# Kernel tuning notes

Measured on AMD Instinct MI355X. Metric: run time of the kernel, lower is better.

## Reference

```python
import jax, jax.numpy as jnp
import numpy as np
from jax.ops import segment_sum

NUM_HEADS = 16
NEG_INF = -jnp.inf


def setup_inputs() -> dict:
    key = jax.random.key(0)
    ks = jax.random.split(key, 12)
    D, H = 1024, NUM_HEADS
    SRC, TGT = 2048, 2048
    V, EV = 32000, 2000
    s = 1.0 / np.sqrt(D)
    return {
        "logits": jax.random.normal(ks[0], (TGT, V), jnp.float32),
        "extended_vocab_ids": jax.random.randint(ks[1], (SRC,), 0, V + EV, jnp.int32),
        "src_subtokens": jax.random.normal(ks[2], (SRC, D), jnp.float32),
        "tgt_subtokens": jax.random.normal(ks[3], (TGT, D), jnp.float32),
        "w_q": jax.random.normal(ks[4], (D, D), jnp.float32) * s,
        "b_q": jax.random.normal(ks[5], (D,), jnp.float32) * 0.02,
        "w_k": jax.random.normal(ks[6], (D, D), jnp.float32) * s,
        "b_k": jax.random.normal(ks[7], (D,), jnp.float32) * 0.02,
        "w_ptr": jax.random.normal(ks[8], (D,), jnp.float32) * s,
        "b_ptr": jax.random.normal(ks[9], (1,), jnp.float32) * 0.02,
        "len_vocab": V,
        "len_extended_vocab": EV,
    }


def _mha_attention(query, key, w_q, b_q, w_k, b_k):
    # SimpleMHA.unbatched_forward: project q/k, per-head scaled dot-product
    # softmax over src, mean over heads -> [TGT, SRC]
    TGT, D = query.shape
    SRC = key.shape[0]
    hd = D // NUM_HEADS
    q = (query @ w_q.T + b_q).reshape(TGT, NUM_HEADS, hd)
    k = (key @ w_k.T + b_k).reshape(SRC, NUM_HEADS, hd)
    scores = jnp.einsum("thd,shd->hts", q, k) / jnp.sqrt(jnp.float32(hd))
    attn = jax.nn.softmax(scores, axis=-1)  # [H, TGT, SRC]
    return attn.mean(axis=0)  # [TGT, SRC]


def reference(logits, extended_vocab_ids, src_subtokens, tgt_subtokens,
              w_q, b_q, w_k, b_k, w_ptr, b_ptr, len_vocab, len_extended_vocab):
    total = len_vocab + len_extended_vocab
    eps = jnp.finfo(jnp.float32).eps
    fmin = jnp.finfo(jnp.float32).min

    # copy gate: sigmoid(Linear(tgt)) -> [TGT, 1]
    copy_prob = jax.nn.sigmoid(tgt_subtokens @ w_ptr + b_ptr[0])[:, None]

    # attention distribution over src tokens [TGT, SRC]
    attn = _mha_attention(tgt_subtokens, src_subtokens, w_q, b_q, w_k, b_k)

    # attention @ one-hot(M) == scatter-add of attention columns by vocab id
    attn_vocab = segment_sum(attn.T, extended_vocab_ids, num_segments=total).T  # [TGT, total]
    attn_vocab = jnp.where(attn_vocab == 0, eps, attn_vocab)
    pointer_log_probs = jnp.log(attn_vocab)

    decoder_log_probs = jax.nn.log_softmax(logits, axis=1)
    decoder_log_probs = jnp.pad(decoder_log_probs, ((0, 0), (0, len_extended_vocab)),
                                constant_values=NEG_INF)

    p = jnp.stack([decoder_log_probs + jnp.log(1.0 - copy_prob),
                   pointer_log_probs + jnp.log(copy_prob)])
    p = jnp.where(p == NEG_INF, fmin, p)
    return jax.scipy.special.logsumexp(p, axis=0)
```

## Files before the change

### kernel.cpp

```cpp
#include <hip/hip_runtime.h>

typedef __attribute__((ext_vector_type(8))) short short8;
typedef __attribute__((ext_vector_type(4))) float f32x4;
typedef __attribute__((ext_vector_type(4))) unsigned int u32x4;
typedef unsigned short u16;
typedef unsigned int u32;

#define MFMA16 __builtin_amdgcn_mfma_f32_16x16x32_bf16

static constexpr int TGT = 2048, SRCN = 2048, DIM = 1024, NH = 16;
static constexpr int NV = 32000, NTOT = 34000;
#define FLT_EPS 1.1920928955078125e-07f

__device__ __forceinline__ u16 f2bf(float f) {
  unsigned u = __float_as_uint(f);
  return (u16)((u + 0x7FFFu + ((u >> 16) & 1u)) >> 16);
}

__device__ __forceinline__ int swz8(int row, int seg) {
  return row * 64 + ((seg ^ (row & 7)) << 3);
}

__device__ __forceinline__ void stats_row_body(
    int t, const float* __restrict__ logits, const float* __restrict__ tgt,
    const float* __restrict__ w_ptr, const float* __restrict__ b_ptr,
    float4* __restrict__ rowc, int tid, int lane, int w, float* red) {
  const f32x4* l4 = (const f32x4*)(logits + (size_t)t * NV);
  float e0 = 0.f, e1 = 0.f, e2 = 0.f, e3 = 0.f;
  const f32x4 z4 = {0.f, 0.f, 0.f, 0.f};
#pragma unroll 2
  for (int pk = 0; pk < 8; ++pk) {
    int g0 = pk * 1024 + tid;
    int g1 = g0 + 256, g2 = g0 + 512, g3 = g0 + 768;
    bool d0 = g0 < NV / 4, d1 = g1 < NV / 4, d2 = g2 < NV / 4, d3 = g3 < NV / 4;
    f32x4 v0 = d0 ? l4[g0] : z4;
    f32x4 v1 = d1 ? l4[g1] : z4;
    f32x4 v2 = d2 ? l4[g2] : z4;
    f32x4 v3 = d3 ? l4[g3] : z4;
    float s0 = (__expf(v0.x) + __expf(v0.y)) + (__expf(v0.z) + __expf(v0.w));
    float s1 = (__expf(v1.x) + __expf(v1.y)) + (__expf(v1.z) + __expf(v1.w));
    float s2 = (__expf(v2.x) + __expf(v2.y)) + (__expf(v2.z) + __expf(v2.w));
    float s3 = (__expf(v3.x) + __expf(v3.y)) + (__expf(v3.z) + __expf(v3.w));
    e0 += d0 ? s0 : 0.f;
    e1 += d1 ? s1 : 0.f;
    e2 += d2 ? s2 : 0.f;
    e3 += d3 ? s3 : 0.f;
  }
  float es = (e0 + e1) + (e2 + e3);

  float4 xv = *(const float4*)&tgt[(size_t)t * DIM + tid * 4];
  float4 wv = *(const float4*)&w_ptr[tid * 4];
  float g = (xv.x * wv.x + xv.y * wv.y) + (xv.z * wv.z + xv.w * wv.w);
  for (int d = 1; d < 64; d <<= 1) {
    es += __shfl_xor(es, d, 64);
    g += __shfl_xor(g, d, 64);
  }
  if (lane == 0) { red[w] = es; red[4 + w] = g; }
  __syncthreads();
  if (tid == 0) {
    float tot = red[0] + red[1] + red[2] + red[3];
    float gs = red[4] + red[5] + red[6] + red[7] + b_ptr[0];
    float c = 1.0f / (1.0f + __expf(-gs));
    float4 rc;
    rc.x = (1.0f - c) / tot;
    rc.y = c * FLT_EPS;
    rc.z = c;
    rc.w = 0.f;
    rowc[t] = rc;
  }
}

__device__ __forceinline__ void sort_body(
    const int* __restrict__ ids, int* __restrict__ sperm,
    u32* __restrict__ segmap, u32* __restrict__ ustart,
    int tid, int lane, int w, char* smem) {
  int* kk_ = (int*)smem;
  int* vv_ = (int*)(smem + 8192);
  int* scan = (int*)(smem + 16384);
  for (int i = tid; i < 2048; i += 256) { kk_[i] = ids[i]; vv_[i] = i; }
  for (int i = tid; i < 2048; i += 256) ustart[i] = 0xFFFFFFFFu;
  if (tid == 0) scan[4] = 0;
  __syncthreads();
  for (int kk = 2; kk <= 2048; kk <<= 1)
    for (int j = kk >> 1; j > 0; j >>= 1) {
      for (int m = tid; m < 1024; m += 256) {
        int i = ((m & ~(j - 1)) << 1) | (m & (j - 1));
        int l = i | j;
        bool asc = ((i & kk) == 0);
        int ki = kk_[i], kl = kk_[l];
        if ((ki > kl) == asc) {
          kk_[i] = kl; kk_[l] = ki;
          int tv = vv_[i]; vv_[i] = vv_[l]; vv_[l] = tv;
        }
      }
      __syncthreads();
    }
  for (int i = tid; i < 2048; i += 256) sperm[i] = vv_[i];
  for (int i = tid; i < NTOT; i += 256) segmap[i] = 0xFFFFFFFFu;
  __syncthreads();
  for (int c = 0; c < 8; ++c) {
    int p = c * 256 + tid;
    int id = kk_[p];
    bool head = (p == 0) || (kk_[p - 1] != id);
    unsigned long long bal = __ballot(head);
    int lanepfx = __popcll(bal & ((1ull << lane) - 1ull));
    int wtot = __popcll(bal);
    if (lane == 0) scan[w] = wtot;
    __syncthreads();
    int woff = 0;
    for (int i = 0; i < w; ++i) woff += scan[i];
    int base = scan[4];
    if (head) {
      int q = p + 1;
      while (q < 2048 && kk_[q] == id) ++q;
      int rank = base + woff + lanepfx;
      u32 cnt = (u32)(q - p);
      segmap[id] = (u32)rank | (cnt << 16);
      ustart[rank] = (u32)p | (cnt << 16);
    }
    __syncthreads();
    if (tid == 0) scan[4] = base + scan[0] + scan[1] + scan[2] + scan[3];
    __syncthreads();
  }
}

__global__ __launch_bounds__(256) void proj_gemm(
    const float* __restrict__ Xq, const float* __restrict__ Wq,
    const float* __restrict__ Bq, u16* __restrict__ Cq,
    const float* __restrict__ Xk, const float* __restrict__ Wk,
    const float* __restrict__ Bk, u16* __restrict__ Ck) {
  const int zz = blockIdx.z;
  const float* X = zz ? Xk : Xq;
  const float* W = zz ? Wk : Wq;
  const float* bias = zz ? Bk : Bq;
  u16* C = zz ? Ck : Cq;
  const float scale = zz ? 1.0f : 0.125f;

  __shared__ u16 As[128 * 32];
  __shared__ u16 Bs[128 * 32];
  const int n0 = blockIdx.x * 128, m0 = blockIdx.y * 128;
  const int tid = threadIdx.x, lane = tid & 63, w = tid >> 6;
  const int wr = w >> 1, wc = w & 1;
  const int srow = tid >> 1, shalf = tid & 1;
  f32x4 acc[4][4] = {};

  for (int k0 = 0; k0 < DIM; k0 += 32) {
    __syncthreads();
    {
      const float* pa = X + (size_t)(m0 + srow) * DIM + k0 + shalf * 16;
      const float* pb = W + (size_t)(n0 + srow) * DIM + k0 + shalf * 16;
      float4 a0 = ((const float4*)pa)[0], a1 = ((const float4*)pa)[1];
      float4 a2 = ((const float4*)pa)[2], a3 = ((const float4*)pa)[3];
      float4 b0 = ((const float4*)pb)[0], b1 = ((const float4*)pb)[1];
      float4 b2 = ((const float4*)pb)[2], b3 = ((const float4*)pb)[3];
      short8 wa0, wa1, wb0, wb1;
      wa0[0]=(short)f2bf(a0.x); wa0[1]=(short)f2bf(a0.y); wa0[2]=(short)f2bf(a0.z); wa0[3]=(short)f2bf(a0.w);
      wa0[4]=(short)f2bf(a1.x); wa0[5]=(short)f2bf(a1.y); wa0[6]=(short)f2bf(a1.z); wa0[7]=(short)f2bf(a1.w);
      wa1[0]=(short)f2bf(a2.x); wa1[1]=(short)f2bf(a2.y); wa1[2]=(short)f2bf(a2.z); wa1[3]=(short)f2bf(a2.w);
      wa1[4]=(short)f2bf(a3.x); wa1[5]=(short)f2bf(a3.y); wa1[6]=(short)f2bf(a3.z); wa1[7]=(short)f2bf(a3.w);
      wb0[0]=(short)f2bf(b0.x); wb0[1]=(short)f2bf(b0.y); wb0[2]=(short)f2bf(b0.z); wb0[3]=(short)f2bf(b0.w);
      wb0[4]=(short)f2bf(b1.x); wb0[5]=(short)f2bf(b1.y); wb0[6]=(short)f2bf(b1.z); wb0[7]=(short)f2bf(b1.w);
      wb1[0]=(short)f2bf(b2.x); wb1[1]=(short)f2bf(b2.y); wb1[2]=(short)f2bf(b2.z); wb1[3]=(short)f2bf(b2.w);
      wb1[4]=(short)f2bf(b3.x); wb1[5]=(short)f2bf(b3.y); wb1[6]=(short)f2bf(b3.z); wb1[7]=(short)f2bf(b3.w);
      int swz = (srow >> 1) & 3;
      int sg0 = ((shalf * 2 + 0) ^ swz) << 3;
      int sg1 = ((shalf * 2 + 1) ^ swz) << 3;
      *(short8*)&As[srow * 32 + sg0] = wa0;
      *(short8*)&As[srow * 32 + sg1] = wa1;
      *(short8*)&Bs[srow * 32 + sg0] = wb0;
      *(short8*)&Bs[srow * 32 + sg1] = wb1;
    }
    __syncthreads();
    const int kq = lane >> 4;
    short8 af[4], bfr[4];
    for (int f = 0; f < 4; ++f) {
      int ar = wr * 64 + f * 16 + (lane & 15);
      af[f] = *(const short8*)&As[ar * 32 + ((kq ^ ((ar >> 1) & 3)) << 3)];
      int br = wc * 64 + f * 16 + (lane & 15);
      bfr[f] = *(const short8*)&Bs[br * 32 + ((kq ^ ((br >> 1) & 3)) << 3)];
    }
    for (int fr = 0; fr < 4; ++fr)
      for (int fc = 0; fc < 4; ++fc)
        acc[fr][fc] = MFMA16(af[fr], bfr[fc], acc[fr][fc], 0, 0, 0);
  }

  for (int fc = 0; fc < 4; ++fc) {
    int col = n0 + wc * 64 + fc * 16 + (lane & 15);
    float bv = bias[col];
    for (int fr = 0; fr < 4; ++fr)
      for (int r = 0; r < 4; ++r) {
        int rowm = m0 + wr * 64 + fr * 16 + ((lane >> 4) << 2) + r;
        C[(size_t)rowm * DIM + col] = f2bf((acc[fr][fc][r] + bv) * scale);
      }
  }
}

__global__ __launch_bounds__(256) void zsum_kernel(const u16* __restrict__ Qb,
                                                   const u16* __restrict__ Kb,
                                                   float* __restrict__ Zinv) {
  __shared__ u16 Ks[64 * 64];
  const int h = blockIdx.x, t0 = blockIdx.y * 64;
  const int tid = threadIdx.x, lane = tid & 63, w = tid >> 6;
  const int arow = t0 + w * 16 + (lane & 15);
  const int acol = h * 64 + ((lane >> 4) << 3);
  short8 a0 = *(const short8*)&Qb[(size_t)arow * DIM + acol];
  short8 a1 = *(const short8*)&Qb[(size_t)arow * DIM + acol + 32];
  float zacc[4] = {0.f, 0.f, 0.f, 0.f};

  for (int s0 = 0; s0 < SRCN; s0 += 64) {
    __syncthreads();
    for (int q = tid; q < 512; q += 256) {
      int r = q >> 3, seg = q & 7;
      *(short8*)&Ks[swz8(r, seg)] = *(const short8*)&Kb[(size_t)(s0 + r) * DIM + h * 64 + seg * 8];
    }
    __syncthreads();
    for (int sub = 0; sub < 4; ++sub) {
      int brow = sub * 16 + (lane & 15);
      int slo = (lane >> 4);
      short8 b0 = *(const short8*)&Ks[swz8(brow, slo)];
      short8 b1 = *(const short8*)&Ks[swz8(brow, slo + 4)];
      f32x4 c = {0.f, 0.f, 0.f, 0.f};
      c = MFMA16(a0, b0, c, 0, 0, 0);
      c = MFMA16(a1, b1, c, 0, 0, 0);
      zacc[0] += __expf(c[0]); zacc[1] += __expf(c[1]);
      zacc[2] += __expf(c[2]); zacc[3] += __expf(c[3]);
    }
  }
  for (int d = 1; d < 16; d <<= 1) {
    zacc[0] += __shfl_xor(zacc[0], d, 64);
    zacc[1] += __shfl_xor(zacc[1], d, 64);
    zacc[2] += __shfl_xor(zacc[2], d, 64);
    zacc[3] += __shfl_xor(zacc[3], d, 64);
  }
  if ((lane & 15) == 0) {
    int trow = t0 + w * 16 + ((lane >> 4) << 2);
    for (int r = 0; r < 4; ++r)
      Zinv[h * TGT + trow + r] = 1.0f / (16.0f * zacc[r]);
  }
}

__global__ __launch_bounds__(256) void fused_mid_kernel(
    const u16* __restrict__ Qb, const u16* __restrict__ Kb,
    const float* __restrict__ Zinv, float* __restrict__ attn,
    const float* __restrict__ logits, const float* __restrict__ tgt,
    const float* __restrict__ w_ptr, const float* __restrict__ b_ptr,
    const int* __restrict__ ids, int* __restrict__ sperm,
    u32* __restrict__ segmap, u32* __restrict__ ustart,
    float4* __restrict__ rowc) {
  __shared__ __align__(16) char smem[20480];
  const int b = blockIdx.x;
  const int tid = threadIdx.x, lane = tid & 63, w = tid >> 6;

  if (b == 0) {
    sort_body(ids, sperm, segmap, ustart, tid, lane, w, smem);
    return;
  }
  if (b > 1024) {
    stats_row_body(b - 1025, logits, tgt, w_ptr, b_ptr, rowc,
                   tid, lane, w, (float*)smem);
    return;
  }
  u16* Qs = (u16*)smem;
  u16* Ks = (u16*)(smem + 8192);
  const int bb = b - 1;
  const int s0 = (bb & 31) * 64, t0 = (bb >> 5) * 64;
  const int wr = w >> 1, wc = w & 1;
  f32x4 acc[2][2] = {};

  for (int h = 0; h < NH; ++h) {
    __syncthreads();
    for (int q = tid; q < 512; q += 256) {
      int r = q >> 3, seg = q & 7;
      *(short8*)&Qs[swz8(r, seg)] = *(const short8*)&Qb[(size_t)(t0 + r) * DIM + h * 64 + seg * 8];
      *(short8*)&Ks[swz8(r, seg)] = *(const short8*)&Kb[(size_t)(s0 + r) * DIM + h * 64 + seg * 8];
    }
    __syncthreads();
    f32x4 sc[2][2] = {};
    for (int kk = 0; kk < 2; ++kk) {
      int seg = (lane >> 4) + kk * 4;
      short8 a0 = *(const short8*)&Qs[swz8(wr * 32 + (lane & 15), seg)];
      short8 a1 = *(const short8*)&Qs[swz8(wr * 32 + 16 + (lane & 15), seg)];
      short8 b0 = *(const short8*)&Ks[swz8(wc * 32 + (lane & 15), seg)];
      short8 b1 = *(const short8*)&Ks[swz8(wc * 32 + 16 + (lane & 15), seg)];
      sc[0][0] = MFMA16(a0, b0, sc[0][0], 0, 0, 0);
      sc[0][1] = MFMA16(a0, b1, sc[0][1], 0, 0, 0);
      sc[1][0] = MFMA16(a1, b0, sc[1][0], 0, 0, 0);
      sc[1][1] = MFMA16(a1, b1, sc[1][1], 0, 0, 0);
    }
    for (int fr = 0; fr < 2; ++fr) {
      int trow = t0 + wr * 32 + fr * 16 + ((lane >> 4) << 2);
      float4 z4 = *(const float4*)&Zinv[h * TGT + trow];
      float iz[4] = {z4.x, z4.y, z4.z, z4.w};
      for (int fc = 0; fc < 2; ++fc)
        for (int r = 0; r < 4; ++r)
          acc[fr][fc][r] += __expf(sc[fr][fc][r]) * iz[r];
    }
  }
  for (int fr = 0; fr < 2; ++fr)
    for (int fc = 0; fc < 2; ++fc)
      for (int r = 0; r < 4; ++r) {
        int t = t0 + wr * 32 + fr * 16 + ((lane >> 4) << 2) + r;
        int s = s0 + wc * 32 + fc * 16 + (lane & 15);
        attn[(size_t)t * SRCN + s] = acc[fr][fc][r];
      }
}

__global__ __launch_bounds__(512) void out_kernel(
    const float* __restrict__ logits, const float4* __restrict__ rowc,
    const int* __restrict__ sperm, const u32* __restrict__ segmap,
    const u32* __restrict__ ustart, const float* __restrict__ attn,
    float* __restrict__ out) {
  __shared__ float aL[2048];
  __shared__ float pL[2048];
  const int t = (TGT - 1) - blockIdx.x;
  const int tid = threadIdx.x;
  float4 rc = rowc[t];
  const float K1 = rc.x, Ceps = rc.y, cc = rc.z;
  const f32x4* l4 = (const f32x4*)(logits + (size_t)t * NV);
  f32x4* o4 = (f32x4*)(out + (size_t)t * NTOT);
  const u32x4* m4 = (const u32x4*)segmap;

  *(float4*)&aL[tid * 4] = *(const float4*)&attn[(size_t)t * SRCN + tid * 4];
  __syncthreads();
  for (int r = tid; r < 2048; r += 512) {
    u32 u = ustart[r];
    if (u != 0xFFFFFFFFu) {
      int p = (int)(u & 0xFFFFu), n = (int)(u >> 16);
      float s = 0.f;
      for (int k = 0; k < n; ++k) s += aL[sperm[p + k]];
      pL[r] = cc * s;
    }
  }
  __syncthreads();

  auto psum = [&](u32 mv) -> float {
    return (mv == 0xFFFFFFFFu) ? Ceps : pL[mv & 0xFFFFu];
  };
  auto elem = [&](float v, bool d, u32 mv) -> float {
    float e = d ? __expf(v) : 0.f;
    return __logf(fmaf(e, K1, psum(mv)));
  };

  const f32x4 z4 = {0.f, 0.f, 0.f, 0.f};
#pragma unroll
  for (int pk = 0; pk < 4; ++pk) {
    int g0 = pk * 2048 + tid;
    int g1 = g0 + 512, g2 = g0 + 1024, g3 = g0 + 1536;
    u32x4 m0 = m4[g0], m1 = m4[g1], m2 = m4[g2], m3 = m4[g3];
    bool d0 = g0 < NV / 4, d1 = g1 < NV / 4, d2 = g2 < NV / 4, d3 = g3 < NV / 4;
    f32x4 v0 = d0 ? __builtin_nontemporal_load(&l4[g0]) : z4;
    f32x4 v1 = d1 ? __builtin_nontemporal_load(&l4[g1]) : z4;
    f32x4 v2 = d2 ? __builtin_nontemporal_load(&l4[g2]) : z4;
    f32x4 v3 = d3 ? __builtin_nontemporal_load(&l4[g3]) : z4;
    f32x4 o0, o1, o2, o3;
    o0.x = elem(v0.x, d0, m0.x); o0.y = elem(v0.y, d0, m0.y);
    o0.z = elem(v0.z, d0, m0.z); o0.w = elem(v0.w, d0, m0.w);
    o1.x = elem(v1.x, d1, m1.x); o1.y = elem(v1.y, d1, m1.y);
    o1.z = elem(v1.z, d1, m1.z); o1.w = elem(v1.w, d1, m1.w);
    o2.x = elem(v2.x, d2, m2.x); o2.y = elem(v2.y, d2, m2.y);
    o2.z = elem(v2.z, d2, m2.z); o2.w = elem(v2.w, d2, m2.w);
    o3.x = elem(v3.x, d3, m3.x); o3.y = elem(v3.y, d3, m3.y);
    o3.z = elem(v3.z, d3, m3.z); o3.w = elem(v3.w, d3, m3.w);
    __builtin_nontemporal_store(o0, &o4[g0]);
    __builtin_nontemporal_store(o1, &o4[g1]);
    __builtin_nontemporal_store(o2, &o4[g2]);
    __builtin_nontemporal_store(o3, &o4[g3]);
  }
  for (int g = 8192 + tid; g < NTOT / 4; g += 512) {
    u32x4 m = m4[g];
    f32x4 o;
    o.x = __logf(psum(m.x));
    o.y = __logf(psum(m.y));
    o.z = __logf(psum(m.z));
    o.w = __logf(psum(m.w));
    __builtin_nontemporal_store(o, &o4[g]);
  }
}

extern "C" void kernel_launch(void* const* d_in, const int* in_sizes, int n_in,
                              void* d_out, int out_size, void* d_ws, size_t ws_size,
                              hipStream_t stream) {
  const float* logits = (const float*)d_in[0];
  const int* ids      = (const int*)d_in[1];
  const float* src    = (const float*)d_in[2];
  const float* tgt    = (const float*)d_in[3];
  const float* w_q    = (const float*)d_in[4];
  const float* b_q    = (const float*)d_in[5];
  const float* w_k    = (const float*)d_in[6];
  const float* b_k    = (const float*)d_in[7];
  const float* w_ptr  = (const float*)d_in[8];
  const float* b_ptr  = (const float*)d_in[9];
  float* out = (float*)d_out;

  char* ws = (char*)d_ws;
  u16* Qb     = (u16*)(ws);
  u16* Kb     = (u16*)(ws + (size_t)4 * 1024 * 1024);
  float* Zinv = (float*)(ws + (size_t)8 * 1024 * 1024);
  float* attn = (float*)(ws + (size_t)8 * 1024 * 1024 + 131072);
  size_t tail_off = (size_t)8 * 1024 * 1024 + 131072 + (size_t)16 * 1024 * 1024;
  int* sperm   = (int*)(ws + tail_off);
  u32* segmap  = (u32*)(ws + tail_off + 8192);
  u32* ustart  = (u32*)(ws + tail_off + 8192 + 136000);
  float4* rowc = (float4*)(ws + tail_off + 8192 + 136000 + 8192);

  proj_gemm<<<dim3(8, 16, 2), 256, 0, stream>>>(tgt, w_q, b_q, Qb, src, w_k, b_k, Kb);
  zsum_kernel<<<dim3(16, 32), 256, 0, stream>>>(Qb, Kb, Zinv);
  fused_mid_kernel<<<3073, 256, 0, stream>>>(Qb, Kb, Zinv, attn, logits, tgt,
                                             w_ptr, b_ptr, ids, sperm, segmap,
                                             ustart, rowc);
  out_kernel<<<TGT, 512, 0, stream>>>(logits, rowc, sperm, segmap, ustart, attn, out);
}
```

Before: 245.7 us.

## Move sort and row-stats blocks into projection GEMM launch

The id sort and per-row logits/copy-gate statistics move out of the attention kernel and into the same launch as the Q/K projection GEMM, as extra blocks. These independent tasks can then overlap the small 256-block GEMM, which leaves most CUs idle, and the attention kernel shrinks to pure attention blocks. Shared memory is reduced to 16KB by reusing the value buffer for the scan scratch, which may improve occupancy. The risk is that the heavy stats blocks delay the GEMM's tail.

```diff
diff --git a/kernel.cpp b/kernel.cpp
--- a/kernel.cpp
+++ b/kernel.cpp
@@ -76,10 +76,8 @@
     int tid, int lane, int w, char* smem) {
   int* kk_ = (int*)smem;
   int* vv_ = (int*)(smem + 8192);
-  int* scan = (int*)(smem + 16384);
   for (int i = tid; i < 2048; i += 256) { kk_[i] = ids[i]; vv_[i] = i; }
   for (int i = tid; i < 2048; i += 256) ustart[i] = 0xFFFFFFFFu;
-  if (tid == 0) scan[4] = 0;
   __syncthreads();
   for (int kk = 2; kk <= 2048; kk <<= 1)
     for (int j = kk >> 1; j > 0; j >>= 1) {
@@ -98,6 +96,9 @@
   for (int i = tid; i < 2048; i += 256) sperm[i] = vv_[i];
   for (int i = tid; i < NTOT; i += 256) segmap[i] = 0xFFFFFFFFu;
   __syncthreads();
+  int* scan = vv_;
+  if (tid == 0) scan[4] = 0;
+  __syncthreads();
   for (int c = 0; c < 8; ++c) {
     int p = c * 256 + tid;
     int id = kk_[p];
@@ -124,22 +125,22 @@
   }
 }
 
-__global__ __launch_bounds__(256) void proj_gemm(
-    const float* __restrict__ Xq, const float* __restrict__ Wq,
+__device__ __forceinline__ void proj_body(
+    int bb, const float* __restrict__ Xq, const float* __restrict__ Wq,
     const float* __restrict__ Bq, u16* __restrict__ Cq,
     const float* __restrict__ Xk, const float* __restrict__ Wk,
-    const float* __restrict__ Bk, u16* __restrict__ Ck) {
-  const int zz = blockIdx.z;
+    const float* __restrict__ Bk, u16* __restrict__ Ck,
+    int tid, int lane, int w, char* smem) {
+  const int zz = bb >> 7;
   const float* X = zz ? Xk : Xq;
   const float* W = zz ? Wk : Wq;
   const float* bias = zz ? Bk : Bq;
   u16* C = zz ? Ck : Cq;
   const float scale = zz ? 1.0f : 0.125f;
 
-  __shared__ u16 As[128 * 32];
-  __shared__ u16 Bs[128 * 32];
-  const int n0 = blockIdx.x * 128, m0 = blockIdx.y * 128;
-  const int tid = threadIdx.x, lane = tid & 63, w = tid >> 6;
+  u16* As = (u16*)smem;
+  u16* Bs = (u16*)(smem + 8192);
+  const int n0 = (bb & 7) * 128, m0 = ((bb >> 3) & 15) * 128;
   const int wr = w >> 1, wc = w & 1;
   const int srow = tid >> 1, shalf = tid & 1;
   f32x4 acc[4][4] = {};
@@ -195,6 +196,29 @@
   }
 }
 
+__global__ __launch_bounds__(256) void fused_a_kernel(
+    const float* __restrict__ logits, const float* __restrict__ tgt,
+    const float* __restrict__ src,
+    const float* __restrict__ w_q, const float* __restrict__ b_q,
+    const float* __restrict__ w_k, const float* __restrict__ b_k,
+    const float* __restrict__ w_ptr, const float* __restrict__ b_ptr,
+    const int* __restrict__ ids,
+    u16* __restrict__ Qb, u16* __restrict__ Kb,
+    int* __restrict__ sperm, u32* __restrict__ segmap,
+    u32* __restrict__ ustart, float4* __restrict__ rowc) {
+  __shared__ __align__(16) char smem[16384];
+  const int b = blockIdx.x;
+  const int tid = threadIdx.x, lane = tid & 63, w = tid >> 6;
+
+  if (b < 256) {
+    proj_body(b, tgt, w_q, b_q, Qb, src, w_k, b_k, Kb, tid, lane, w, smem);
+  } else if (b == 256) {
+    sort_body(ids, sperm, segmap, ustart, tid, lane, w, smem);
+  } else {
+    stats_row_body(b - 257, logits, tgt, w_ptr, b_ptr, rowc, tid, lane, w, (float*)smem);
+  }
+}
+
 __global__ __launch_bounds__(256) void zsum_kernel(const u16* __restrict__ Qb,
                                                    const u16* __restrict__ Kb,
                                                    float* __restrict__ Zinv) {
@@ -239,31 +263,15 @@
   }
 }
 
-__global__ __launch_bounds__(256) void fused_mid_kernel(
+__global__ __launch_bounds__(256) void attn_kernel(
     const u16* __restrict__ Qb, const u16* __restrict__ Kb,
-    const float* __restrict__ Zinv, float* __restrict__ attn,
-    const float* __restrict__ logits, const float* __restrict__ tgt,
-    const float* __restrict__ w_ptr, const float* __restrict__ b_ptr,
-    const int* __restrict__ ids, int* __restrict__ sperm,
-    u32* __restrict__ segmap, u32* __restrict__ ustart,
-    float4* __restrict__ rowc) {
-  __shared__ __align__(16) char smem[20480];
-  const int b = blockIdx.x;
-  const int tid = threadIdx.x, lane = tid & 63, w = tid >> 6;
-
-  if (b == 0) {
-    sort_body(ids, sperm, segmap, ustart, tid, lane, w, smem);
-    return;
-  }
-  if (b > 1024) {
-    stats_row_body(b - 1025, logits, tgt, w_ptr, b_ptr, rowc,
-                   tid, lane, w, (float*)smem);
-    return;
-  }
+    const float* __restrict__ Zinv, float* __restrict__ attn) {
+  __shared__ __align__(16) char smem[16384];
   u16* Qs = (u16*)smem;
   u16* Ks = (u16*)(smem + 8192);
-  const int bb = b - 1;
+  const int bb = blockIdx.x;
   const int s0 = (bb & 31) * 64, t0 = (bb >> 5) * 64;
+  const int tid = threadIdx.x, lane = tid & 63, w = tid >> 6;
   const int wr = w >> 1, wc = w & 1;
   f32x4 acc[2][2] = {};
 
@@ -403,10 +411,10 @@
   u32* ustart  = (u32*)(ws + tail_off + 8192 + 136000);
   float4* rowc = (float4*)(ws + tail_off + 8192 + 136000 + 8192);
 
-  proj_gemm<<<dim3(8, 16, 2), 256, 0, stream>>>(tgt, w_q, b_q, Qb, src, w_k, b_k, Kb);
+  fused_a_kernel<<<2305, 256, 0, stream>>>(logits, tgt, src, w_q, b_q, w_k, b_k,
+                                           w_ptr, b_ptr, ids, Qb, Kb,
+                                           sperm, segmap, ustart, rowc);
   zsum_kernel<<<dim3(16, 32), 256, 0, stream>>>(Qb, Kb, Zinv);
-  fused_mid_kernel<<<3073, 256, 0, stream>>>(Qb, Kb, Zinv, attn, logits, tgt,
-                                             w_ptr, b_ptr, ids, sperm, segmap,
-                                             ustart, rowc);
+  attn_kernel<<<1024, 256, 0, stream>>>(Qb, Kb, Zinv, attn);
   out_kernel<<<TGT, 512, 0, stream>>>(logits, rowc, sperm, segmap, ustart, attn, out);
 }
```

Measured after the change: 225.5 us, median of 2. -8.2%, faster.
